# Performance work log

Hardware: AMD Instinct MI355X
Metric: run time of the kernel (lower is better)

Reference implementation:

```python
import jax, jax.numpy as jnp
import numpy as np

N = 50000
E = 800000
IN_FEAT = 128
HIDDEN = 64
HEADS = 4
CLASSES = 40
NEG_SLOPE = 0.2


def setup_inputs() -> dict:
    key = jax.random.key(0)
    ks = jax.random.split(key, 12)
    x = jax.random.normal(ks[0], (N, IN_FEAT), dtype=jnp.float32)
    # edge_index without self loops (module removes then re-adds them)
    src = jax.random.randint(ks[1], (E,), 0, N)
    off = jax.random.randint(ks[2], (E,), 1, N)
    dst = (src + off) % N  # guaranteed dst != src
    edge_index = jnp.stack([src, dst]).astype(jnp.int64)
    g = 1.0 / np.sqrt(IN_FEAT)
    lin1_w = jax.random.normal(ks[3], (IN_FEAT, HEADS * HIDDEN), dtype=jnp.float32) * g
    lin1_b = jax.random.normal(ks[4], (HEADS * HIDDEN,), dtype=jnp.float32) * 0.01
    att1 = jax.random.normal(ks[5], (1, HEADS, 2 * HIDDEN), dtype=jnp.float32) * (1.0 / np.sqrt(2 * HIDDEN))
    bias1 = jnp.zeros((HEADS * HIDDEN,), dtype=jnp.float32)
    lin2_w = jax.random.normal(ks[6], (HEADS * HIDDEN, CLASSES), dtype=jnp.float32) * (1.0 / np.sqrt(HEADS * HIDDEN))
    lin2_b = jax.random.normal(ks[7], (CLASSES,), dtype=jnp.float32) * 0.01
    att2 = jax.random.normal(ks[8], (1, 1, 2 * CLASSES), dtype=jnp.float32) * (1.0 / np.sqrt(2 * CLASSES))
    bias2 = jnp.zeros((CLASSES,), dtype=jnp.float32)
    return {"x": x, "edge_index": edge_index, "lin1_w": lin1_w, "lin1_b": lin1_b,
            "att1": att1, "bias1": bias1, "lin2_w": lin2_w, "lin2_b": lin2_b,
            "att2": att2, "bias2": bias2}


def gat_conv(x, src, dst, W, b_lin, att, bias, heads, oc):
    n = x.shape[0]
    fea = (x @ W + b_lin).reshape(n, heads, oc)            # [N, H, C]
    # attention logits: (cat([x_i, x_j]) * att).sum(-1) decomposed per node
    score_i = jnp.einsum('nhc,hc->nh', fea, att[0, :, :oc])  # target half
    score_j = jnp.einsum('nhc,hc->nh', fea, att[0, :, oc:])  # source half
    alpha = score_i[dst] + score_j[src]                    # [E, H]
    alpha = jax.nn.leaky_relu(alpha, NEG_SLOPE)
    # segment softmax over target node
    amax = jax.ops.segment_max(alpha, dst, num_segments=n)
    alpha = jnp.exp(alpha - amax[dst])
    asum = jax.ops.segment_sum(alpha, dst, num_segments=n)
    alpha = alpha / (asum[dst] + 1e-16)
    # message = x_j * alpha; scatter-add to target
    msg = fea[src] * alpha[:, :, None]                     # [E, H, C]
    out = jax.ops.segment_sum(msg, dst, num_segments=n)
    return out.reshape(n, heads * oc) + bias               # concat=True


def reference(x, edge_index, lin1_w, lin1_b, att1, bias1, lin2_w, lin2_b, att2, bias2):
    n = x.shape[0]
    loop = jnp.arange(n, dtype=edge_index.dtype)
    src = jnp.concatenate([edge_index[0], loop])  # add self loops
    dst = jnp.concatenate([edge_index[1], loop])
    h = gat_conv(x, src, dst, lin1_w, lin1_b, att1, bias1, HEADS, HIDDEN)
    h = jax.nn.relu(h)
    h = gat_conv(h, src, dst, lin2_w, lin2_b, att2, bias2, 1, CLASSES)
    return jax.nn.softmax(h, axis=1)
```

## Files before the change

kernel.cpp:

```cpp
#include <hip/hip_runtime.h>
#include <hip/hip_fp16.h>

#define NN 50000
#define NE 800000
#define INFEAT 128
#define F1 256
#define HID 64
#define CLS 40
#define NEGS 0.2f
#define CAP 48
#define GBM 128
#define GB1 1564
#define HB4 782

__device__ __forceinline__ float lrelu(float x) { return x > 0.0f ? x : NEGS * x; }

struct alignas(8) H4 { __half2 a, b; };

typedef __attribute__((ext_vector_type(8))) _Float16 f16x8;
typedef __attribute__((ext_vector_type(4))) float f32x4;

__global__ __launch_bounds__(256) void gemm1_hist_k(const float* __restrict__ A,
                                                    const float* __restrict__ W,
                                                    const float* __restrict__ b,
                                                    const float* __restrict__ att1,
                                                    __half* __restrict__ feah,
                                                    float* __restrict__ sI,
                                                    float* __restrict__ sJ,
                                                    const int* __restrict__ dst,
                                                    int* __restrict__ cnt,
                                                    int* __restrict__ ord) {
    __shared__ __align__(16) _Float16 As[128][40];
    __shared__ __align__(16) _Float16 Ws[4][64][40];
    int bx = blockIdx.x;
    int tid = threadIdx.x;
    if (bx < HB4) {
        int base = bx * 1024 + tid;
        int e0 = base, e1 = base + 256, e2 = base + 512, e3 = base + 768;
        if (e0 < NE) ord[e0] = atomicAdd(&cnt[dst[e0]], 1);
        if (e1 < NE) ord[e1] = atomicAdd(&cnt[dst[e1]], 1);
        if (e2 < NE) ord[e2] = atomicAdd(&cnt[dst[e2]], 1);
        if (e3 < NE) ord[e3] = atomicAdd(&cnt[dst[e3]], 1);
        return;
    }
    int gb = bx - HB4;
    int wid = tid >> 6, lane = tid & 63;
    int row0 = (gb >> 2) * GBM;
    int head = gb & 3;
    int colB = head * 64;
    int lr = lane & 15;
    int lg = lane >> 4;

    for (int q = tid; q < 1024; q += 256) {
        int col = q & 63;
        int kg  = (q >> 6) & 3;
        int ks  = q >> 8;
        f16x8 wv;
        #pragma unroll
        for (int j = 0; j < 8; ++j)
            wv[j] = (_Float16)W[(size_t)(ks * 32 + kg * 8 + j) * F1 + colB + col];
        *(f16x8*)&Ws[ks][col][kg * 8] = wv;
    }

    f32x4 acc[2][4];
    #pragma unroll
    for (int rt = 0; rt < 2; ++rt)
        #pragma unroll
        for (int ct = 0; ct < 4; ++ct) acc[rt][ct] = (f32x4){0.f, 0.f, 0.f, 0.f};

    for (int ks = 0; ks < 4; ++ks) {
        int k0 = ks * 32;
        #pragma unroll
        for (int i = 0; i < 2; ++i) {
            int q = tid + 256 * i;
            int r = q >> 2;
            int c8 = (q & 3) * 8;
            int grow = row0 + r;
            f16x8 hv;
            if (grow < NN) {
                float4 v0 = *(const float4*)&A[(size_t)grow * INFEAT + k0 + c8];
                float4 v1 = *(const float4*)&A[(size_t)grow * INFEAT + k0 + c8 + 4];
                hv[0] = (_Float16)v0.x; hv[1] = (_Float16)v0.y;
                hv[2] = (_Float16)v0.z; hv[3] = (_Float16)v0.w;
                hv[4] = (_Float16)v1.x; hv[5] = (_Float16)v1.y;
                hv[6] = (_Float16)v1.z; hv[7] = (_Float16)v1.w;
            } else {
                #pragma unroll
                for (int j = 0; j < 8; ++j) hv[j] = (_Float16)0.f;
            }
            *(f16x8*)&As[r][c8] = hv;
        }
        __syncthreads();
        f16x8 afrag[2], bfrag[4];
        #pragma unroll
        for (int rt = 0; rt < 2; ++rt)
            afrag[rt] = *(const f16x8*)&As[wid * 32 + rt * 16 + lr][lg * 8];
        #pragma unroll
        for (int ct = 0; ct < 4; ++ct)
            bfrag[ct] = *(const f16x8*)&Ws[ks][ct * 16 + lr][lg * 8];
        #pragma unroll
        for (int rt = 0; rt < 2; ++rt)
            #pragma unroll
            for (int ct = 0; ct < 4; ++ct)
                acc[rt][ct] = __builtin_amdgcn_mfma_f32_16x16x32_f16(
                    afrag[rt], bfrag[ct], acc[rt][ct], 0, 0, 0);
        __syncthreads();
    }
    float aIv[4], aJv[4], bv[4];
    #pragma unroll
    for (int ct = 0; ct < 4; ++ct) {
        int cin = ct * 16 + lr;
        aIv[ct] = att1[head * 2 * HID + cin];
        aJv[ct] = att1[head * 2 * HID + HID + cin];
        bv[ct]  = b[colB + cin];
    }
    #pragma unroll
    for (int rt = 0; rt < 2; ++rt) {
        #pragma unroll
        for (int i = 0; i < 4; ++i) {
            int grow = row0 + wid * 32 + rt * 16 + lg * 4 + i;
            float o[4];
            float sIp = 0.f, sJp = 0.f;
            #pragma unroll
            for (int ct = 0; ct < 4; ++ct) {
                o[ct] = acc[rt][ct][i] + bv[ct];
                sIp += o[ct] * aIv[ct];
                sJp += o[ct] * aJv[ct];
            }
            #pragma unroll
            for (int off = 1; off < 16; off <<= 1) {
                sIp += __shfl_xor(sIp, off);
                sJp += __shfl_xor(sJp, off);
            }
            if (grow < NN) {
                #pragma unroll
                for (int ct = 0; ct < 4; ++ct)
                    feah[(size_t)grow * F1 + colB + ct * 16 + lr] = __float2half(o[ct]);
                if (lr == 0) {
                    sI[grow * 4 + head] = sIp;
                    sJ[grow * 4 + head] = sJp;
                }
            }
        }
    }
}

#define EF_T (NE / 2)
__global__ void ep_fill_k(const int* __restrict__ src, const int* __restrict__ dst,
                          const int* __restrict__ ord,
                          const float* __restrict__ sI, const float* __restrict__ sJ,
                          int* __restrict__ csr, float4* __restrict__ ep4) {
    int t = blockIdx.x * blockDim.x + threadIdx.x;
    if (t >= EF_T) return;
    int e0 = t, e1 = t + EF_T;
    int s0 = src[e0], s1 = src[e1];
    int d0 = dst[e0], d1 = dst[e1];
    int t0 = ord[e0], t1 = ord[e1];
    t0 = t0 < CAP ? t0 : CAP - 1;
    t1 = t1 < CAP ? t1 : CAP - 1;
    int p0 = d0 * CAP + t0, p1 = d1 * CAP + t1;
    float4 si0 = *(const float4*)&sI[d0 * 4];
    float4 si1 = *(const float4*)&sI[d1 * 4];
    float4 sj0 = *(const float4*)&sJ[s0 * 4];
    float4 sj1 = *(const float4*)&sJ[s1 * 4];
    float4 r0, r1;
    r0.x = __expf(lrelu(si0.x + sj0.x)); r0.y = __expf(lrelu(si0.y + sj0.y));
    r0.z = __expf(lrelu(si0.z + sj0.z)); r0.w = __expf(lrelu(si0.w + sj0.w));
    r1.x = __expf(lrelu(si1.x + sj1.x)); r1.y = __expf(lrelu(si1.y + sj1.y));
    r1.z = __expf(lrelu(si1.z + sj1.z)); r1.w = __expf(lrelu(si1.w + sj1.w));
    csr[p0] = s0; csr[p1] = s1;
    ep4[p0] = r0; ep4[p1] = r1;
}

__global__ __launch_bounds__(256, 6) void agg1_k(const __half* __restrict__ feah,
                                                 const float* __restrict__ sI,
                                                 const float* __restrict__ sJ,
                                                 const float* __restrict__ epf,
                                                 const int* __restrict__ cnt,
                                                 const int* __restrict__ csr,
                                                 const float* __restrict__ bias,
                                                 __half* __restrict__ out) {
    int wid = threadIdx.x >> 6, lane = threadIdx.x & 63;
    int n = blockIdx.x * 4 + wid;
    if (n >= NN) return;
    int h = lane >> 4;
    int c = lane * 4;
    float p = __expf(lrelu(sI[n * 4 + h] + sJ[n * 4 + h]));
    float asum = p;
    H4 vs = *(const H4*)&feah[(size_t)n * F1 + c];
    float2 sx = __half22float2(vs.a), sy = __half22float2(vs.b);
    float4 acc = make_float4(sx.x * p, sx.y * p, sy.x * p, sy.y * p);
    int beg = n * CAP;
    int m = cnt[n]; if (m > CAP) m = CAP;
    int end = beg + m;
    int e = beg;
    for (; e + 8 <= end; e += 8) {
        int s0 = csr[e + 0], s1 = csr[e + 1], s2 = csr[e + 2], s3 = csr[e + 3];
        int s4 = csr[e + 4], s5 = csr[e + 5], s6 = csr[e + 6], s7 = csr[e + 7];
        float p0 = epf[(e + 0) * 4 + h], p1 = epf[(e + 1) * 4 + h];
        float p2 = epf[(e + 2) * 4 + h], p3 = epf[(e + 3) * 4 + h];
        float p4 = epf[(e + 4) * 4 + h], p5 = epf[(e + 5) * 4 + h];
        float p6 = epf[(e + 6) * 4 + h], p7 = epf[(e + 7) * 4 + h];
        H4 v0 = *(const H4*)&feah[(size_t)s0 * F1 + c];
        H4 v1 = *(const H4*)&feah[(size_t)s1 * F1 + c];
        H4 v2 = *(const H4*)&feah[(size_t)s2 * F1 + c];
        H4 v3 = *(const H4*)&feah[(size_t)s3 * F1 + c];
        H4 v4 = *(const H4*)&feah[(size_t)s4 * F1 + c];
        H4 v5 = *(const H4*)&feah[(size_t)s5 * F1 + c];
        H4 v6 = *(const H4*)&feah[(size_t)s6 * F1 + c];
        H4 v7 = *(const H4*)&feah[(size_t)s7 * F1 + c];
        asum += ((p0 + p1) + (p2 + p3)) + ((p4 + p5) + (p6 + p7));
        float2 x0 = __half22float2(v0.a), y0 = __half22float2(v0.b);
        float2 x1 = __half22float2(v1.a), y1 = __half22float2(v1.b);
        float2 x2 = __half22float2(v2.a), y2 = __half22float2(v2.b);
        float2 x3 = __half22float2(v3.a), y3 = __half22float2(v3.b);
        float2 x4 = __half22float2(v4.a), y4 = __half22float2(v4.b);
        float2 x5 = __half22float2(v5.a), y5 = __half22float2(v5.b);
        float2 x6 = __half22float2(v6.a), y6 = __half22float2(v6.b);
        float2 x7 = __half22float2(v7.a), y7 = __half22float2(v7.b);
        acc.x += (x0.x * p0 + x1.x * p1 + x2.x * p2 + x3.x * p3)
               + (x4.x * p4 + x5.x * p5 + x6.x * p6 + x7.x * p7);
        acc.y += (x0.y * p0 + x1.y * p1 + x2.y * p2 + x3.y * p3)
               + (x4.y * p4 + x5.y * p5 + x6.y * p6 + x7.y * p7);
        acc.z += (y0.x * p0 + y1.x * p1 + y2.x * p2 + y3.x * p3)
               + (y4.x * p4 + y5.x * p5 + y6.x * p6 + y7.x * p7);
        acc.w += (y0.y * p0 + y1.y * p1 + y2.y * p2 + y3.y * p3)
               + (y4.y * p4 + y5.y * p5 + y6.y * p6 + y7.y * p7);
    }
    for (; e + 4 <= end; e += 4) {
        int s0 = csr[e], s1 = csr[e + 1], s2 = csr[e + 2], s3 = csr[e + 3];
        float p0 = epf[(e + 0) * 4 + h], p1 = epf[(e + 1) * 4 + h];
        float p2 = epf[(e + 2) * 4 + h], p3 = epf[(e + 3) * 4 + h];
        H4 v0 = *(const H4*)&feah[(size_t)s0 * F1 + c];
        H4 v1 = *(const H4*)&feah[(size_t)s1 * F1 + c];
        H4 v2 = *(const H4*)&feah[(size_t)s2 * F1 + c];
        H4 v3 = *(const H4*)&feah[(size_t)s3 * F1 + c];
        asum += (p0 + p1) + (p2 + p3);
        float2 x0 = __half22float2(v0.a), y0 = __half22float2(v0.b);
        float2 x1 = __half22float2(v1.a), y1 = __half22float2(v1.b);
        float2 x2 = __half22float2(v2.a), y2 = __half22float2(v2.b);
        float2 x3 = __half22float2(v3.a), y3 = __half22float2(v3.b);
        acc.x += x0.x * p0 + x1.x * p1 + x2.x * p2 + x3.x * p3;
        acc.y += x0.y * p0 + x1.y * p1 + x2.y * p2 + x3.y * p3;
        acc.z += y0.x * p0 + y1.x * p1 + y2.x * p2 + y3.x * p3;
        acc.w += y0.y * p0 + y1.y * p1 + y2.y * p2 + y3.y * p3;
    }
    for (; e < end; ++e) {
        int s = csr[e];
        float pe = epf[e * 4 + h];
        asum += pe;
        H4 v = *(const H4*)&feah[(size_t)s * F1 + c];
        float2 x = __half22float2(v.a), y = __half22float2(v.b);
        acc.x += x.x * pe; acc.y += x.y * pe;
        acc.z += y.x * pe; acc.w += y.y * pe;
    }
    float inv = 1.0f / (asum + 1e-16f);
    float4 bv = *(const float4*)&bias[c];
    H4 o4;
    o4.a = __floats2half2_rn(fmaxf(acc.x * inv + bv.x, 0.f),
                             fmaxf(acc.y * inv + bv.y, 0.f));
    o4.b = __floats2half2_rn(fmaxf(acc.z * inv + bv.z, 0.f),
                             fmaxf(acc.w * inv + bv.w, 0.f));
    *(H4*)&out[(size_t)n * F1 + c] = o4;
}

#define G2M 128
__global__ __launch_bounds__(256) void gemm2_k(const __half* __restrict__ h1h,
                                               const float* __restrict__ W2,
                                               const float* __restrict__ b2,
                                               const float* __restrict__ att2,
                                               __half* __restrict__ fea2h,
                                               float* __restrict__ s2I,
                                               float* __restrict__ s2J) {
    __shared__ __align__(16) _Float16 Ws2[48][264];
    __shared__ __align__(16) _Float16 As2[128][40];
    int tid = threadIdx.x;
    int wid = tid >> 6, lane = tid & 63;
    int lr = lane & 15, lg = lane >> 4;
    int row0 = blockIdx.x * G2M;
    for (int q = tid; q < 48 * 32; q += 256) {
        int col = q >> 5;
        int kg  = q & 31;
        f16x8 wv;
        #pragma unroll
        for (int j = 0; j < 8; ++j) {
            int k = kg * 8 + j;
            wv[j] = (col < CLS) ? (_Float16)W2[(size_t)k * CLS + col] : (_Float16)0.f;
        }
        *(f16x8*)&Ws2[col][kg * 8] = wv;
    }
    f32x4 acc[2][3];
    #pragma unroll
    for (int rt = 0; rt < 2; ++rt)
        #pragma unroll
        for (int ct = 0; ct < 3; ++ct) acc[rt][ct] = (f32x4){0.f, 0.f, 0.f, 0.f};

    for (int k0 = 0; k0 < F1; k0 += 32) {
        #pragma unroll
        for (int i = 0; i < 2; ++i) {
            int q = tid + 256 * i;
            int r = q >> 2;
            int c8 = (q & 3) * 8;
            int grow = row0 + r;
            f16x8 v;
            if (grow < NN) v = *(const f16x8*)&h1h[(size_t)grow * F1 + k0 + c8];
            else {
                #pragma unroll
                for (int j = 0; j < 8; ++j) v[j] = (_Float16)0.f;
            }
            *(f16x8*)&As2[r][c8] = v;
        }
        __syncthreads();
        f16x8 af[2], bf[3];
        #pragma unroll
        for (int rt = 0; rt < 2; ++rt)
            af[rt] = *(const f16x8*)&As2[wid * 32 + rt * 16 + lr][lg * 8];
        #pragma unroll
        for (int ct = 0; ct < 3; ++ct)
            bf[ct] = *(const f16x8*)&Ws2[ct * 16 + lr][k0 + lg * 8];
        #pragma unroll
        for (int rt = 0; rt < 2; ++rt)
            #pragma unroll
            for (int ct = 0; ct < 3; ++ct)
                acc[rt][ct] = __builtin_amdgcn_mfma_f32_16x16x32_f16(
                    af[rt], bf[ct], acc[rt][ct], 0, 0, 0);
        __syncthreads();
    }
    float bcol[3], aIc[3], aJc[3];
    bool valid[3];
    #pragma unroll
    for (int ct = 0; ct < 3; ++ct) {
        int col = ct * 16 + lr;
        valid[ct] = col < CLS;
        int cc = valid[ct] ? col : 0;
        bcol[ct] = b2[cc];
        aIc[ct] = valid[ct] ? att2[cc] : 0.f;
        aJc[ct] = valid[ct] ? att2[CLS + cc] : 0.f;
    }
    #pragma unroll
    for (int rt = 0; rt < 2; ++rt) {
        #pragma unroll
        for (int i = 0; i < 4; ++i) {
            int grow = row0 + wid * 32 + rt * 16 + lg * 4 + i;
            float o[3];
            float sIp = 0.f, sJp = 0.f;
            #pragma unroll
            for (int ct = 0; ct < 3; ++ct) {
                o[ct] = acc[rt][ct][i] + bcol[ct];
                sIp += o[ct] * aIc[ct];
                sJp += o[ct] * aJc[ct];
            }
            #pragma unroll
            for (int off = 1; off < 16; off <<= 1) {
                sIp += __shfl_xor(sIp, off);
                sJp += __shfl_xor(sJp, off);
            }
            if (grow < NN) {
                #pragma unroll
                for (int ct = 0; ct < 3; ++ct)
                    if (valid[ct])
                        fea2h[(size_t)grow * CLS + ct * 16 + lr] = __float2half(o[ct]);
                if (lr == 0) {
                    s2I[grow] = sIp;
                    s2J[grow] = sJp;
                }
            }
        }
    }
}

__global__ __launch_bounds__(256) void agg2_k(const __half* __restrict__ fea2h,
                                              const float* __restrict__ s2I,
                                              const float* __restrict__ s2J,
                                              const int* __restrict__ cnt,
                                              const int* __restrict__ csr,
                                              const float* __restrict__ bias2,
                                              float* __restrict__ out) {
    int wid = threadIdx.x >> 6, lane = threadIdx.x & 63;
    int n = blockIdx.x * 4 + wid;
    if (n >= NN) return;
    float si = s2I[n], sjn = s2J[n];
    int c = lane < CLS ? lane : 0;
    float p = __expf(lrelu(si + sjn));
    float asum = p;
    float acc = __half2float(fea2h[(size_t)n * CLS + c]) * p;
    int beg = n * CAP;
    int m = cnt[n]; if (m > CAP) m = CAP;
    int end = beg + m;
    int e = beg;
    for (; e + 8 <= end; e += 8) {
        int s0 = csr[e + 0], s1 = csr[e + 1], s2 = csr[e + 2], s3 = csr[e + 3];
        int s4 = csr[e + 4], s5 = csr[e + 5], s6 = csr[e + 6], s7 = csr[e + 7];
        float a0 = s2J[s0], a1 = s2J[s1], a2 = s2J[s2], a3 = s2J[s3];
        float a4 = s2J[s4], a5 = s2J[s5], a6 = s2J[s6], a7 = s2J[s7];
        __half f0 = fea2h[(size_t)s0 * CLS + c];
        __half f1 = fea2h[(size_t)s1 * CLS + c];
        __half f2 = fea2h[(size_t)s2 * CLS + c];
        __half f3 = fea2h[(size_t)s3 * CLS + c];
        __half f4 = fea2h[(size_t)s4 * CLS + c];
        __half f5 = fea2h[(size_t)s5 * CLS + c];
        __half f6 = fea2h[(size_t)s6 * CLS + c];
        __half f7 = fea2h[(size_t)s7 * CLS + c];
        float p0 = __expf(lrelu(si + a0));
        float p1 = __expf(lrelu(si + a1));
        float p2 = __expf(lrelu(si + a2));
        float p3 = __expf(lrelu(si + a3));
        float p4 = __expf(lrelu(si + a4));
        float p5 = __expf(lrelu(si + a5));
        float p6 = __expf(lrelu(si + a6));
        float p7 = __expf(lrelu(si + a7));
        asum += ((p0 + p1) + (p2 + p3)) + ((p4 + p5) + (p6 + p7));
        acc += (__half2float(f0) * p0 + __half2float(f1) * p1
              + __half2float(f2) * p2 + __half2float(f3) * p3)
             + (__half2float(f4) * p4 + __half2float(f5) * p5
              + __half2float(f6) * p6 + __half2float(f7) * p7);
    }
    for (; e + 4 <= end; e += 4) {
        int s0 = csr[e], s1 = csr[e + 1], s2 = csr[e + 2], s3 = csr[e + 3];
        float p0 = __expf(lrelu(si + s2J[s0]));
        float p1 = __expf(lrelu(si + s2J[s1]));
        float p2 = __expf(lrelu(si + s2J[s2]));
        float p3 = __expf(lrelu(si + s2J[s3]));
        __half f0 = fea2h[(size_t)s0 * CLS + c];
        __half f1 = fea2h[(size_t)s1 * CLS + c];
        __half f2 = fea2h[(size_t)s2 * CLS + c];
        __half f3 = fea2h[(size_t)s3 * CLS + c];
        asum += (p0 + p1) + (p2 + p3);
        acc += __half2float(f0) * p0 + __half2float(f1) * p1
             + __half2float(f2) * p2 + __half2float(f3) * p3;
    }
    for (; e < end; ++e) {
        int s = csr[e];
        float pe = __expf(lrelu(si + s2J[s]));
        asum += pe;
        acc += __half2float(fea2h[(size_t)s * CLS + c]) * pe;
    }
    float row = acc / (asum + 1e-16f) + bias2[c];
    float v = (lane < CLS) ? row : -3.0e38f;
    float vm = v;
    #pragma unroll
    for (int off = 32; off; off >>= 1) vm = fmaxf(vm, __shfl_xor(vm, off));
    float ex = (lane < CLS) ? __expf(v - vm) : 0.f;
    float es = ex;
    #pragma unroll
    for (int off = 32; off; off >>= 1) es += __shfl_xor(es, off);
    if (lane < CLS) out[(size_t)n * CLS + lane] = ex / es;
}

extern "C" void kernel_launch(void* const* d_in, const int* in_sizes, int n_in,
                              void* d_out, int out_size, void* d_ws, size_t ws_size,
                              hipStream_t stream) {
    const float* x     = (const float*)d_in[0];
    const int*   ei    = (const int*)d_in[1];
    const float* w1    = (const float*)d_in[2];
    const float* b1    = (const float*)d_in[3];
    const float* att1  = (const float*)d_in[4];
    const float* bias1 = (const float*)d_in[5];
    const float* w2    = (const float*)d_in[6];
    const float* b2    = (const float*)d_in[7];
    const float* att2  = (const float*)d_in[8];
    const float* bias2 = (const float*)d_in[9];
    const int* src = ei;
    const int* dst = ei + NE;
    float* out = (float*)d_out;

    char* p = (char*)d_ws;
    auto alloc = [&](size_t bytes) {
        char* r = p;
        p += (bytes + 255) & ~(size_t)255;
        return r;
    };
    __half* fea1h = (__half*)alloc((size_t)NN * F1 * 2);
    __half* h1h   = (__half*)alloc((size_t)NN * F1 * 2);
    float* sI1    = (float*)alloc((size_t)NN * 4 * 4);
    float* sJ1    = (float*)alloc((size_t)NN * 4 * 4);
    __half* fea2h = (__half*)alloc((size_t)NN * CLS * 2);
    float* s2I    = (float*)alloc((size_t)NN * 4);
    float* s2J    = (float*)alloc((size_t)NN * 4);
    int*   cnt    = (int*)alloc((size_t)NN * 4);
    int*   ord    = (int*)alloc((size_t)NE * 4);
    int*   csr    = (int*)alloc((size_t)NN * CAP * 4);
    float* ep1    = (float*)alloc((size_t)NN * CAP * 4 * 4);

    hipMemsetAsync(cnt, 0, (size_t)NN * 4, stream);

    gemm1_hist_k<<<HB4 + GB1, 256, 0, stream>>>(x, w1, b1, att1, fea1h, sI1, sJ1,
                                                dst, cnt, ord);
    ep_fill_k<<<(EF_T + 255) / 256, 256, 0, stream>>>(src, dst, ord, sI1, sJ1,
                                                      csr, (float4*)ep1);
    agg1_k<<<(NN + 3) / 4, 256, 0, stream>>>(fea1h, sI1, sJ1, ep1, cnt, csr, bias1, h1h);
    gemm2_k<<<(NN + G2M - 1) / G2M, 256, 0, stream>>>(h1h, w2, b2, att2, fea2h, s2I, s2J);
    agg2_k<<<(NN + 3) / 4, 256, 0, stream>>>(fea2h, s2I, s2J, cnt, csr, bias2, out);
}
```

Before: 215.9 us.

## Replicate degree histogram counters and widen GEMM1 blocks to all heads

The in-degree histogram now uses 8 replicated counter arrays, chosen by block index, to reduce atomic contention. A new base_k kernel prefix-sums the replicas into per-node offsets and the total count, and ep_fill decodes the packed replica/slot value to find each edge's CSR slot. Separately, each GEMM1 block now computes all 256 output columns (4 heads) for its 128 rows instead of one head per block. This cuts redundant loads of A, at the cost of more accumulator registers and an extra kernel launch plus a larger memset.

```diff
diff --git a/kernel.cpp b/kernel.cpp
--- a/kernel.cpp
+++ b/kernel.cpp
@@ -10,7 +10,7 @@
 #define NEGS 0.2f
 #define CAP 48
 #define GBM 128
-#define GB1 1564
+#define GB1 391
 #define HB4 782
 
 __device__ __forceinline__ float lrelu(float x) { return x > 0.0f ? x : NEGS * x; }
@@ -28,45 +28,34 @@
                                                     float* __restrict__ sI,
                                                     float* __restrict__ sJ,
                                                     const int* __restrict__ dst,
-                                                    int* __restrict__ cnt,
+                                                    int* __restrict__ cnt8,
                                                     int* __restrict__ ord) {
     __shared__ __align__(16) _Float16 As[128][40];
-    __shared__ __align__(16) _Float16 Ws[4][64][40];
+    __shared__ __align__(16) _Float16 Ws[256][40];
     int bx = blockIdx.x;
     int tid = threadIdx.x;
     if (bx < HB4) {
+        int rep = bx & 7;
+        int* cr = cnt8 + rep * NN;
         int base = bx * 1024 + tid;
         int e0 = base, e1 = base + 256, e2 = base + 512, e3 = base + 768;
-        if (e0 < NE) ord[e0] = atomicAdd(&cnt[dst[e0]], 1);
-        if (e1 < NE) ord[e1] = atomicAdd(&cnt[dst[e1]], 1);
-        if (e2 < NE) ord[e2] = atomicAdd(&cnt[dst[e2]], 1);
-        if (e3 < NE) ord[e3] = atomicAdd(&cnt[dst[e3]], 1);
+        if (e0 < NE) ord[e0] = (rep << 26) | atomicAdd(&cr[dst[e0]], 1);
+        if (e1 < NE) ord[e1] = (rep << 26) | atomicAdd(&cr[dst[e1]], 1);
+        if (e2 < NE) ord[e2] = (rep << 26) | atomicAdd(&cr[dst[e2]], 1);
+        if (e3 < NE) ord[e3] = (rep << 26) | atomicAdd(&cr[dst[e3]], 1);
         return;
     }
     int gb = bx - HB4;
     int wid = tid >> 6, lane = tid & 63;
-    int row0 = (gb >> 2) * GBM;
-    int head = gb & 3;
-    int colB = head * 64;
+    int row0 = gb * GBM;
     int lr = lane & 15;
     int lg = lane >> 4;
 
-    for (int q = tid; q < 1024; q += 256) {
-        int col = q & 63;
-        int kg  = (q >> 6) & 3;
-        int ks  = q >> 8;
-        f16x8 wv;
-        #pragma unroll
-        for (int j = 0; j < 8; ++j)
-            wv[j] = (_Float16)W[(size_t)(ks * 32 + kg * 8 + j) * F1 + colB + col];
-        *(f16x8*)&Ws[ks][col][kg * 8] = wv;
-    }
-
-    f32x4 acc[2][4];
+    f32x4 acc[2][16];
     #pragma unroll
     for (int rt = 0; rt < 2; ++rt)
         #pragma unroll
-        for (int ct = 0; ct < 4; ++ct) acc[rt][ct] = (f32x4){0.f, 0.f, 0.f, 0.f};
+        for (int ct = 0; ct < 16; ++ct) acc[rt][ct] = (f32x4){0.f, 0.f, 0.f, 0.f};
 
     for (int ks = 0; ks < 4; ++ks) {
         int k0 = ks * 32;
@@ -90,64 +79,91 @@
             }
             *(f16x8*)&As[r][c8] = hv;
         }
+        #pragma unroll
+        for (int kg = 0; kg < 4; ++kg) {
+            f16x8 wv;
+            #pragma unroll
+            for (int j = 0; j < 8; ++j)
+                wv[j] = (_Float16)W[(size_t)(k0 + kg * 8 + j) * F1 + tid];
+            *(f16x8*)&Ws[tid][kg * 8] = wv;
+        }
         __syncthreads();
-        f16x8 afrag[2], bfrag[4];
+        f16x8 afrag[2];
         #pragma unroll
         for (int rt = 0; rt < 2; ++rt)
             afrag[rt] = *(const f16x8*)&As[wid * 32 + rt * 16 + lr][lg * 8];
         #pragma unroll
-        for (int ct = 0; ct < 4; ++ct)
-            bfrag[ct] = *(const f16x8*)&Ws[ks][ct * 16 + lr][lg * 8];
-        #pragma unroll
-        for (int rt = 0; rt < 2; ++rt)
-            #pragma unroll
-            for (int ct = 0; ct < 4; ++ct)
-                acc[rt][ct] = __builtin_amdgcn_mfma_f32_16x16x32_f16(
-                    afrag[rt], bfrag[ct], acc[rt][ct], 0, 0, 0);
+        for (int ct = 0; ct < 16; ++ct) {
+            f16x8 bf = *(const f16x8*)&Ws[ct * 16 + lr][lg * 8];
+            acc[0][ct] = __builtin_amdgcn_mfma_f32_16x16x32_f16(afrag[0], bf, acc[0][ct], 0, 0, 0);
+            acc[1][ct] = __builtin_amdgcn_mfma_f32_16x16x32_f16(afrag[1], bf, acc[1][ct], 0, 0, 0);
+        }
         __syncthreads();
     }
-    float aIv[4], aJv[4], bv[4];
-    #pragma unroll
-    for (int ct = 0; ct < 4; ++ct) {
-        int cin = ct * 16 + lr;
-        aIv[ct] = att1[head * 2 * HID + cin];
-        aJv[ct] = att1[head * 2 * HID + HID + cin];
-        bv[ct]  = b[colB + cin];
+    float bv[16], aIv[16], aJv[16];
+    #pragma unroll
+    for (int ct = 0; ct < 16; ++ct) {
+        int col = ct * 16 + lr;
+        int h = col >> 6, cin = col & 63;
+        bv[ct]  = b[col];
+        aIv[ct] = att1[h * 2 * HID + cin];
+        aJv[ct] = att1[h * 2 * HID + HID + cin];
     }
     #pragma unroll
     for (int rt = 0; rt < 2; ++rt) {
         #pragma unroll
         for (int i = 0; i < 4; ++i) {
             int grow = row0 + wid * 32 + rt * 16 + lg * 4 + i;
-            float o[4];
-            float sIp = 0.f, sJp = 0.f;
+            float o[16];
+            float sIp[4] = {0.f, 0.f, 0.f, 0.f};
+            float sJp[4] = {0.f, 0.f, 0.f, 0.f};
             #pragma unroll
-            for (int ct = 0; ct < 4; ++ct) {
+            for (int ct = 0; ct < 16; ++ct) {
                 o[ct] = acc[rt][ct][i] + bv[ct];
-                sIp += o[ct] * aIv[ct];
-                sJp += o[ct] * aJv[ct];
+                int h = ct >> 2;
+                sIp[h] += o[ct] * aIv[ct];
+                sJp[h] += o[ct] * aJv[ct];
             }
             #pragma unroll
             for (int off = 1; off < 16; off <<= 1) {
-                sIp += __shfl_xor(sIp, off);
-                sJp += __shfl_xor(sJp, off);
+                #pragma unroll
+                for (int h = 0; h < 4; ++h) {
+                    sIp[h] += __shfl_xor(sIp[h], off);
+                    sJp[h] += __shfl_xor(sJp[h], off);
+                }
             }
             if (grow < NN) {
                 #pragma unroll
-                for (int ct = 0; ct < 4; ++ct)
-                    feah[(size_t)grow * F1 + colB + ct * 16 + lr] = __float2half(o[ct]);
+                for (int ct = 0; ct < 16; ++ct)
+                    feah[(size_t)grow * F1 + ct * 16 + lr] = __float2half(o[ct]);
                 if (lr == 0) {
-                    sI[grow * 4 + head] = sIp;
-                    sJ[grow * 4 + head] = sJp;
+                    #pragma unroll
+                    for (int h = 0; h < 4; ++h) {
+                        sI[grow * 4 + h] = sIp[h];
+                        sJ[grow * 4 + h] = sJp[h];
+                    }
                 }
             }
         }
     }
+}
+
+__global__ void base_k(const int* __restrict__ cnt8, int* __restrict__ base8,
+                       int* __restrict__ cnt) {
+    int n = blockIdx.x * 256 + threadIdx.x;
+    if (n >= NN) return;
+    int s = 0;
+    int bb[8];
+    #pragma unroll
+    for (int r = 0; r < 8; ++r) { bb[r] = s; s += cnt8[r * NN + n]; }
+    cnt[n] = s;
+    *(int4*)&base8[n * 8]     = make_int4(bb[0], bb[1], bb[2], bb[3]);
+    *(int4*)&base8[n * 8 + 4] = make_int4(bb[4], bb[5], bb[6], bb[7]);
 }
 
 #define EF_T (NE / 2)
 __global__ void ep_fill_k(const int* __restrict__ src, const int* __restrict__ dst,
-                          const int* __restrict__ ord,
+                          const int* __restrict__ ord, const int* __restrict__ base8,
                           const float* __restrict__ sI, const float* __restrict__ sJ,
                           int* __restrict__ csr, float4* __restrict__ ep4) {
     int t = blockIdx.x * blockDim.x + threadIdx.x;
@@ -155,7 +171,9 @@
     int e0 = t, e1 = t + EF_T;
     int s0 = src[e0], s1 = src[e1];
     int d0 = dst[e0], d1 = dst[e1];
-    int t0 = ord[e0], t1 = ord[e1];
+    int o0 = ord[e0], o1 = ord[e1];
+    int t0 = base8[d0 * 8 + (o0 >> 26)] + (o0 & 0x3FFFFFF);
+    int t1 = base8[d1 * 8 + (o1 >> 26)] + (o1 & 0x3FFFFFF);
     t0 = t0 < CAP ? t0 : CAP - 1;
     t1 = t1 < CAP ? t1 : CAP - 1;
     int p0 = d0 * CAP + t0, p1 = d1 * CAP + t1;
@@ -477,16 +495,19 @@
     __half* fea2h = (__half*)alloc((size_t)NN * CLS * 2);
     float* s2I    = (float*)alloc((size_t)NN * 4);
     float* s2J    = (float*)alloc((size_t)NN * 4);
+    int*   cnt8   = (int*)alloc((size_t)8 * NN * 4);
+    int*   base8  = (int*)alloc((size_t)NN * 8 * 4);
     int*   cnt    = (int*)alloc((size_t)NN * 4);
     int*   ord    = (int*)alloc((size_t)NE * 4);
     int*   csr    = (int*)alloc((size_t)NN * CAP * 4);
     float* ep1    = (float*)alloc((size_t)NN * CAP * 4 * 4);
 
-    hipMemsetAsync(cnt, 0, (size_t)NN * 4, stream);
+    hipMemsetAsync(cnt8, 0, (size_t)8 * NN * 4, stream);
 
     gemm1_hist_k<<<HB4 + GB1, 256, 0, stream>>>(x, w1, b1, att1, fea1h, sI1, sJ1,
-                                                dst, cnt, ord);
-    ep_fill_k<<<(EF_T + 255) / 256, 256, 0, stream>>>(src, dst, ord, sI1, sJ1,
+                                                dst, cnt8, ord);
+    base_k<<<(NN + 255) / 256, 256, 0, stream>>>(cnt8, base8, cnt);
+    ep_fill_k<<<(EF_T + 255) / 256, 256, 0, stream>>>(src, dst, ord, base8, sI1, sJ1,
                                                       csr, (float4*)ep1);
     agg1_k<<<(NN + 3) / 4, 256, 0, stream>>>(fea1h, sI1, sJ1, ep1, cnt, csr, bias1, h1h);
     gemm2_k<<<(NN + G2M - 1) / G2M, 256, 0, stream>>>(h1h, w2, b2, att2, fea2h, s2I, s2J);
```

New measurement: 224.4 us. 1.04x slower.
